# Optimization experiments

Measured on AMD Instinct MI355X. Metric: run time of the kernel, lower is better.

## Reference

```python
import jax, jax.numpy as jnp
import numpy as np

N, L, D = 2, 2048, 96
H, DK, DV = 4, 16, 16
OUT = 96
SPATIAL = H * (3 + 1 + 3)  # points + distance + direction per head
INF = 100000.0
EPS_DIR = 1e-10
EPS_LN = 1e-5


def setup_inputs() -> dict:
    key = jax.random.key(0)
    ks = jax.random.split(key, 10)
    return {
        "x": jax.random.normal(ks[0], (N, L, D), jnp.float32),
        "pos_CA": jax.random.normal(ks[1], (N, L, 3), jnp.float32),
        "pos_CB": jax.random.normal(ks[2], (N, L, 3), jnp.float32),
        "frame": jax.random.normal(ks[3], (N, L, 3, 3), jnp.float32),
        "mask": jnp.ones((N, L), dtype=bool),
        "Wq": jax.random.normal(ks[4], (D, H * DK), jnp.float32) * 0.1,
        "Wk": jax.random.normal(ks[5], (D, H * DK), jnp.float32) * 0.1,
        "Wv": jax.random.normal(ks[6], (D, H * DV), jnp.float32) * 0.1,
        "Wo": jax.random.normal(ks[7], (H * DV + SPATIAL, OUT), jnp.float32) * 0.1,
        "bo": jnp.zeros((OUT,), jnp.float32),
        "gamma": jnp.ones((OUT,), jnp.float32),
        "beta": jnp.zeros((OUT,), jnp.float32),
    }


def reference(x, pos_CA, pos_CB, frame, mask, Wq, Wk, Wv, Wo, bo, gamma, beta):
    n, l, _ = x.shape
    q = (x @ Wq).reshape(n, l, H, DK)
    k = (x @ Wk).reshape(n, l, H, DK)
    v = (x @ Wv).reshape(n, l, H, DV)

    # logits (N, L_q, L_k, H)
    logits = jnp.einsum('blhd,bkhd->blkh', q, k)
    mask_row = mask[:, :, None, None]           # (N, L, 1, 1)
    mask_pair = mask_row & mask[:, None, :, None]
    logits = jnp.where(mask_pair, logits, logits - INF)
    alpha = jax.nn.softmax(logits, axis=2)
    alpha = jnp.where(mask_row, alpha, 0.0)

    feat_node = jnp.einsum('blkh,bkhd->blhd', alpha, v).reshape(n, l, H * DV)

    # rel_pos[b,l,k] = CB[k] - CA[l]
    rel_pos = pos_CB[:, None, :, :] - pos_CA[:, :, None, :]
    atom_pos_bias = jnp.einsum('blkh,blkd->blhd', alpha, rel_pos)  # (N,L,H,3)
    feat_distance = jnp.linalg.norm(atom_pos_bias, axis=-1, keepdims=True)
    feat_points = jnp.einsum('blij,blhj->blhi', frame, atom_pos_bias)
    feat_direction = feat_points / (jnp.linalg.norm(feat_points, axis=-1, keepdims=True) + EPS_DIR)

    feat_spatial = jnp.concatenate([
        feat_points.reshape(n, l, H * 3),
        feat_distance.reshape(n, l, H),
        feat_direction.reshape(n, l, H * 3),
    ], axis=-1)

    feat_all = jnp.concatenate([feat_node, feat_spatial], axis=-1) @ Wo + bo
    feat_all = jnp.where(mask[:, :, None], feat_all, 0.0)

    # output_dim == input_dim -> residual + LayerNorm
    h = x + feat_all
    mu = jnp.mean(h, axis=-1, keepdims=True)
    var = jnp.var(h, axis=-1, keepdims=True)
    return (h - mu) / jnp.sqrt(var + EPS_LN) * gamma + beta
```

## Files before the change

### kernel.cpp

```cpp
#include <hip/hip_runtime.h>
#include <hip/hip_fp16.h>

typedef _Float16 f16;
typedef _Float16 v8h __attribute__((ext_vector_type(8)));
typedef short    v4s __attribute__((ext_vector_type(4)));
typedef short    v8s __attribute__((ext_vector_type(8)));
typedef float    v4f __attribute__((ext_vector_type(4)));

#define NB   2
#define LSEQ 2048
#define DIM  96
#define NH   4
#define ROWS 4096
#define NT16 128
#define NT32 64
#define OUTD 96
#define SHIFT 12.0f
#define ST 28
#define PART_STRIDE 320

#define MFMA_F16(A, B, C)  __builtin_amdgcn_mfma_f32_16x16x32_f16((A), (B), (C), 0, 0, 0)
#define MFMA_BF16(A, B, C) __builtin_amdgcn_mfma_f32_16x16x32_bf16((A), (B), (C), 0, 0, 0)

static __device__ __forceinline__ short f2bf(float f) {
    unsigned u = __builtin_bit_cast(unsigned, f);
    u += 0x7FFF + ((u >> 16) & 1);
    return (short)(u >> 16);
}

__global__ __launch_bounds__(256) void proj_kernel(
    const float* __restrict__ x,
    const float* __restrict__ posCB,
    const float* __restrict__ Wq,
    const float* __restrict__ Wk,
    const float* __restrict__ Wv,
    f16*   __restrict__ qc,
    f16*   __restrict__ kc,
    short* __restrict__ vf,
    short* __restrict__ pf)
{
    const int t    = threadIdx.x;
    const int w    = t >> 6;
    const int lane = t & 63;
    const int tile = blockIdx.x / 3;
    const int role = blockIdx.x - tile * 3;
    const int b    = tile >> 7;
    const int t16  = tile & 127;
    const int row0 = b * LSEQ + t16 * 16;
    const int h    = lane >> 4, d = lane & 15;

    __shared__ float xs[16 * DIM];
    __shared__ float Wl[DIM * 64];
    __shared__ short stage[4][264];

    const float* Wsel = (role == 0) ? Wq : (role == 1) ? Wk : Wv;
    {
        const float* src = x + (size_t)row0 * DIM;
        #pragma unroll
        for (int i = 0; i < 6; ++i)  xs[t + 256 * i] = src[t + 256 * i];
        #pragma unroll
        for (int i = 0; i < 24; ++i) Wl[t + 256 * i] = Wsel[t + 256 * i];
    }
    __syncthreads();

    float acc[4] = {0.f, 0.f, 0.f, 0.f};
    #pragma unroll 8
    for (int dd = 0; dd < DIM; ++dd) {
        const float wv = Wl[dd * 64 + lane];
        #pragma unroll
        for (int r = 0; r < 4; ++r)
            acc[r] = fmaf(xs[(w * 4 + r) * DIM + dd], wv, acc[r]);
    }

    if (role < 2) {
        #pragma unroll
        for (int r = 0; r < 4; ++r) {
            const int m = w * 4 + r;
            const int idx = (m + 16 * (d >> 3)) * 8 + (d & 7);
            stage[h][idx] = __builtin_bit_cast(short, (f16)acc[r]);
        }
    } else {
        #pragma unroll
        for (int r = 0; r < 4; ++r) {
            const int m = w * 4 + r;
            const int idx = (d + 16 * (m >> 3)) * 8 + (m & 7);
            stage[h][idx] = f2bf(acc[r]);
        }
    }
    __syncthreads();

    const int bh = b * NH + w;
    const v4s val = *(v4s*)(void*)&stage[w][lane * 4];
    if (role == 0)
        *(v4s*)(void*)(qc + ((size_t)(bh * NT16 + t16)) * 256 + lane * 4) = val;
    else if (role == 1)
        *(v4s*)(void*)(kc + ((size_t)(bh * NT16 + t16)) * 256 + lane * 4) = val;
    else
        *(v4s*)(vf + ((size_t)(bh * NT32 + (t16 >> 1))) * 512 + (t16 & 1) * 256 + lane * 4) = val;

    if (blockIdx.x < NB * NT32) {
        const int b2 = blockIdx.x >> 6, t2 = blockIdx.x & 63;
        const int lf = t & 63, jh = t >> 6;
        const int n = lf & 15, kq = lf >> 4;
        #pragma unroll
        for (int u = 0; u < 2; ++u) {
            const int key = t2 * 32 + kq * 8 + jh * 2 + u;
            float val2 = 0.f;
            if (n < 3)       val2 = posCB[((size_t)(b2 * LSEQ + key)) * 3 + n];
            else if (n == 3) val2 = 1.f;
            pf[((size_t)(b2 * NT32 + t2)) * 512 + lf * 8 + jh * 2 + u] = f2bf(val2);
        }
    }
}

__global__ __launch_bounds__(512, 1) void attn_kernel(
    const f16*   __restrict__ qc,
    const f16*   __restrict__ kc,
    const short* __restrict__ vf,
    const short* __restrict__ pf,
    float*       __restrict__ part)
{
    const int w     = threadIdx.x >> 6;
    const int lane  = threadIdx.x & 63;
    const int head  = w & 3, khalf = w >> 2;
    const int b     = blockIdx.x >> 9;
    const int qt    = (blockIdx.x >> 2) & 127;
    const int kq    = blockIdx.x & 3;
    const int bh    = b * NH + head;
    const int quad  = lane >> 4, c16 = lane & 15;

    __shared__ short pT[8][32 * ST];

    v8h aq = {0,0,0,0,0,0,0,0};
    if (lane < 32)
        aq = *(const v8h*)(qc + ((size_t)(bh * NT16 + qt)) * 256 + lane * 8);
    const f16*   kb = kc + (size_t)bh * NT16 * 256;
    const short* vb = vf + (size_t)bh * NT32 * 512;
    const short* pb = pf + (size_t)b  * NT32 * 512;

    v4f O  = {0.f, 0.f, 0.f, 0.f};
    v4f Wa = {0.f, 0.f, 0.f, 0.f};
    const v4f zero = {0.f, 0.f, 0.f, 0.f};
    float srow[4] = {0.f, 0.f, 0.f, 0.f};
    short* slot = pT[w];

    #pragma unroll 2
    for (int i = 0; i < 8; ++i) {
        const int t32 = kq * 16 + khalf * 8 + i;
        v8h bk0 = {0,0,0,0,0,0,0,0}, bk1 = {0,0,0,0,0,0,0,0};
        if (lane < 32) {
            bk0 = *(const v8h*)(kb + (size_t)(2 * t32    ) * 256 + lane * 8);
            bk1 = *(const v8h*)(kb + (size_t)(2 * t32 + 1) * 256 + lane * 8);
        }
        v4f S0 = MFMA_F16(aq, bk0, zero);
        v4f S1 = MFMA_F16(aq, bk1, zero);

        v4s pr0, pr1;
        #pragma unroll
        for (int r = 0; r < 4; ++r) {
            const float e0 = __expf(S0[r] - SHIFT);
            const float e1 = __expf(S1[r] - SHIFT);
            pr0[r] = f2bf(e0);
            pr1[r] = f2bf(e1);
            srow[r] += e0 + e1;
        }

        *(v4s*)(slot + c16 * ST + quad * 4)        = pr0;
        *(v4s*)(slot + (16 + c16) * ST + quad * 4) = pr1;
        v8s ap;
        #pragma unroll
        for (int j = 0; j < 8; ++j)
            ap[j] = slot[(quad * 8 + j) * ST + c16];

        const v8s bv = *(const v8s*)(vb + (size_t)t32 * 512 + lane * 8);
        O = MFMA_BF16(ap, bv, O);
        const v8s bp = *(const v8s*)(pb + (size_t)t32 * 512 + lane * 8);
        Wa = MFMA_BF16(ap, bp, Wa);
    }

    #pragma unroll
    for (int mask = 1; mask < 16; mask <<= 1) {
        #pragma unroll
        for (int r = 0; r < 4; ++r) srow[r] += __shfl_xor(srow[r], mask);
    }

    const int combo = kq * 2 + khalf;
    float* dst = part + ((((size_t)(b * 128 + qt)) * 8 + combo) * 4 + head) * PART_STRIDE;
    *(v4f*)(dst + lane * 4) = O;
    if (c16 < 3) {
        #pragma unroll
        for (int r = 0; r < 4; ++r)
            dst[256 + (4 * quad + r) * 3 + c16] = Wa[r];
    }
    if (c16 == 3) {
        #pragma unroll
        for (int r = 0; r < 4; ++r) dst[304 + 4 * quad + r] = srow[r];
    }
}

__global__ __launch_bounds__(512) void epi_kernel(
    const float* __restrict__ part,
    const float* __restrict__ x,
    const float* __restrict__ posCA,
    const float* __restrict__ frame,
    const float* __restrict__ Wo,
    const float* __restrict__ bo,
    const float* __restrict__ gamma,
    const float* __restrict__ beta,
    float*       __restrict__ out)
{
    const int w    = threadIdx.x >> 6;
    const int lane = threadIdx.x & 63;
    const int b    = blockIdx.x >> 7;
    const int qt   = blockIdx.x & 127;
    const int quad = lane >> 4, c16 = lane & 15;

    __shared__ float feat[16][100];
    __shared__ float aps[16][NH][3];

    if (w < 4) {
        const float* pbase =
            part + (((size_t)(b * 128 + qt)) * 8 * 4 + w) * PART_STRIDE;
        v4f O = {0.f, 0.f, 0.f, 0.f};
        float wa[4] = {0.f, 0.f, 0.f, 0.f};
        float sr[4] = {0.f, 0.f, 0.f, 0.f};
        #pragma unroll
        for (int combo = 0; combo < 8; ++combo) {
            const float* pp = pbase + (size_t)combo * 4 * PART_STRIDE;
            O += *(const v4f*)(pp + lane * 4);
            if (c16 < 3) {
                #pragma unroll
                for (int r = 0; r < 4; ++r)
                    wa[r] += pp[256 + (4 * quad + r) * 3 + c16];
            }
            #pragma unroll
            for (int r = 0; r < 4; ++r) sr[r] += pp[304 + 4 * quad + r];
        }
        float inv[4];
        #pragma unroll
        for (int r = 0; r < 4; ++r) inv[r] = 1.f / sr[r];
        #pragma unroll
        for (int r = 0; r < 4; ++r)
            feat[4 * quad + r][w * 16 + c16] = O[r] * inv[r];
        if (c16 < 3) {
            #pragma unroll
            for (int r = 0; r < 4; ++r)
                aps[4 * quad + r][w][c16] = wa[r] * inv[r];
        }
    }
    __syncthreads();

    const int rowg0 = b * LSEQ + qt * 16;

    if (lane < 8) {
        const int pair = w * 8 + lane;
        const int r16 = pair >> 2, hh = pair & 3;
        const int grow = rowg0 + r16;
        float apb[3];
        #pragma unroll
        for (int j = 0; j < 3; ++j)
            apb[j] = aps[r16][hh][j] - posCA[(size_t)grow * 3 + j];
        const float dist = sqrtf(apb[0]*apb[0] + apb[1]*apb[1] + apb[2]*apb[2]);
        float fp[3];
        #pragma unroll
        for (int i = 0; i < 3; ++i) {
            float a = 0.f;
            #pragma unroll
            for (int j = 0; j < 3; ++j)
                a = fmaf(frame[(size_t)grow * 9 + i * 3 + j], apb[j], a);
            fp[i] = a;
        }
        const float fpn  = sqrtf(fp[0]*fp[0] + fp[1]*fp[1] + fp[2]*fp[2]);
        const float rinv = 1.f / (fpn + 1e-10f);
        #pragma unroll
        for (int i = 0; i < 3; ++i) {
            feat[r16][64 + hh * 3 + i] = fp[i];
            feat[r16][80 + hh * 3 + i] = fp[i] * rinv;
        }
        feat[r16][76 + hh] = dist;
    }
    __syncthreads();

    #pragma unroll
    for (int rr = 0; rr < 2; ++rr) {
        const int r16 = w * 2 + rr;
        const int grow = rowg0 + r16;

        float acc0 = bo[lane];
        #pragma unroll 4
        for (int r2 = 0; r2 < 92; ++r2)
            acc0 = fmaf(feat[r16][r2], Wo[r2 * OUTD + lane], acc0);
        const float hv0 = acc0 + x[(size_t)grow * DIM + lane];

        float hv1 = 0.f;
        if (lane < 32) {
            float acc1 = bo[64 + lane];
            #pragma unroll 4
            for (int r2 = 0; r2 < 92; ++r2)
                acc1 = fmaf(feat[r16][r2], Wo[r2 * OUTD + 64 + lane], acc1);
            hv1 = acc1 + x[(size_t)grow * DIM + 64 + lane];
        }

        float ls = hv0 + hv1;
        float lq = fmaf(hv0, hv0, hv1 * hv1);
        #pragma unroll
        for (int off = 32; off > 0; off >>= 1) {
            ls += __shfl_xor(ls, off);
            lq += __shfl_xor(lq, off);
        }
        const float mu  = ls * (1.f / OUTD);
        const float var = lq * (1.f / OUTD) - mu * mu;
        const float rs  = rsqrtf(var + 1e-5f);

        out[(size_t)grow * OUTD + lane] = (hv0 - mu) * rs * gamma[lane] + beta[lane];
        if (lane < 32)
            out[(size_t)grow * OUTD + 64 + lane] =
                (hv1 - mu) * rs * gamma[64 + lane] + beta[64 + lane];
    }
}

extern "C" void kernel_launch(void* const* d_in, const int* in_sizes, int n_in,
                              void* d_out, int out_size, void* d_ws, size_t ws_size,
                              hipStream_t stream)
{
    const float* x     = (const float*)d_in[0];
    const float* posCA = (const float*)d_in[1];
    const float* posCB = (const float*)d_in[2];
    const float* frame = (const float*)d_in[3];
    const float* Wq    = (const float*)d_in[5];
    const float* Wk    = (const float*)d_in[6];
    const float* Wv    = (const float*)d_in[7];
    const float* Wo    = (const float*)d_in[8];
    const float* bo    = (const float*)d_in[9];
    const float* gamma = (const float*)d_in[10];
    const float* beta  = (const float*)d_in[11];

    f16*   qc   = (f16*)d_ws;
    f16*   kc   = qc + (size_t)8 * NT16 * 256;
    short* vf   = (short*)(kc + (size_t)8 * NT16 * 256);
    short* pf   = vf + (size_t)8 * NT32 * 512;
    float* part = (float*)(pf + (size_t)NB * NT32 * 512);

    proj_kernel<<<256 * 3, 256, 0, stream>>>(x, posCB, Wq, Wk, Wv, qc, kc, vf, pf);
    attn_kernel<<<NB * NT16 * 4, 512, 0, stream>>>(qc, kc, vf, pf, part);
    epi_kernel<<<NB * NT16, 512, 0, stream>>>(part, x, posCA, frame,
                                              Wo, bo, gamma, beta,
                                              (float*)d_out);
}
```

Measured before the change: 123.9 us.

## Interleave K tile layout, vectorize staging loads, truncate exp to bf16

The projection kernel now loads x and the weight matrix into shared memory as float4 instead of scalar floats. K is stored in an interleaved 32-key layout, so each lane fetches both 16-key halves with one contiguous 32-byte read instead of two strided reads. The exp-to-bf16 conversion in attention becomes a truncating bit shift, and the row sum uses the same truncated values so the normalization matches the weights actually fed to the MFMA. The truncation drops round-to-nearest, which slightly changes numerics.

```diff
diff --git a/kernel.cpp b/kernel.cpp
--- a/kernel.cpp
+++ b/kernel.cpp
@@ -6,6 +6,7 @@
 typedef short    v4s __attribute__((ext_vector_type(4)));
 typedef short    v8s __attribute__((ext_vector_type(8)));
 typedef float    v4f __attribute__((ext_vector_type(4)));
+typedef unsigned int u32;
 
 #define NB   2
 #define LSEQ 2048
@@ -55,11 +56,12 @@
 
     const float* Wsel = (role == 0) ? Wq : (role == 1) ? Wk : Wv;
     {
-        const float* src = x + (size_t)row0 * DIM;
-        #pragma unroll
-        for (int i = 0; i < 6; ++i)  xs[t + 256 * i] = src[t + 256 * i];
-        #pragma unroll
-        for (int i = 0; i < 24; ++i) Wl[t + 256 * i] = Wsel[t + 256 * i];
+        const float4* src = (const float4*)(x + (size_t)row0 * DIM);
+        ((float4*)xs)[t] = src[t];
+        if (t < 128) ((float4*)xs)[256 + t] = src[256 + t];
+        const float4* ws4 = (const float4*)Wsel;
+        #pragma unroll
+        for (int i = 0; i < 6; ++i) ((float4*)Wl)[t + 256 * i] = ws4[t + 256 * i];
     }
     __syncthreads();
 
@@ -93,9 +95,10 @@
     const v4s val = *(v4s*)(void*)&stage[w][lane * 4];
     if (role == 0)
         *(v4s*)(void*)(qc + ((size_t)(bh * NT16 + t16)) * 256 + lane * 4) = val;
-    else if (role == 1)
-        *(v4s*)(void*)(kc + ((size_t)(bh * NT16 + t16)) * 256 + lane * 4) = val;
-    else
+    else if (role == 1) {
+        *(v4s*)(void*)(kc + ((size_t)(bh * NT32 + (t16 >> 1))) * 512
+                          + (lane >> 1) * 16 + (t16 & 1) * 8 + (lane & 1) * 4) = val;
+    } else
         *(v4s*)(vf + ((size_t)(bh * NT32 + (t16 >> 1))) * 512 + (t16 & 1) * 256 + lane * 4) = val;
 
     if (blockIdx.x < NB * NT32) {
@@ -134,7 +137,7 @@
     v8h aq = {0,0,0,0,0,0,0,0};
     if (lane < 32)
         aq = *(const v8h*)(qc + ((size_t)(bh * NT16 + qt)) * 256 + lane * 8);
-    const f16*   kb = kc + (size_t)bh * NT16 * 256;
+    const f16*   kb = kc + (size_t)bh * NT32 * 512;
     const short* vb = vf + (size_t)bh * NT32 * 512;
     const short* pb = pf + (size_t)b  * NT32 * 512;
 
@@ -149,8 +152,9 @@
         const int t32 = kq * 16 + khalf * 8 + i;
         v8h bk0 = {0,0,0,0,0,0,0,0}, bk1 = {0,0,0,0,0,0,0,0};
         if (lane < 32) {
-            bk0 = *(const v8h*)(kb + (size_t)(2 * t32    ) * 256 + lane * 8);
-            bk1 = *(const v8h*)(kb + (size_t)(2 * t32 + 1) * 256 + lane * 8);
+            const f16* kp = kb + (size_t)t32 * 512 + lane * 16;
+            bk0 = *(const v8h*)(kp);
+            bk1 = *(const v8h*)(kp + 8);
         }
         v4f S0 = MFMA_F16(aq, bk0, zero);
         v4f S1 = MFMA_F16(aq, bk1, zero);
@@ -158,11 +162,12 @@
         v4s pr0, pr1;
         #pragma unroll
         for (int r = 0; r < 4; ++r) {
-            const float e0 = __expf(S0[r] - SHIFT);
-            const float e1 = __expf(S1[r] - SHIFT);
-            pr0[r] = f2bf(e0);
-            pr1[r] = f2bf(e1);
-            srow[r] += e0 + e1;
+            const u32 a0 = __builtin_bit_cast(u32, __expf(S0[r] - SHIFT));
+            const u32 a1 = __builtin_bit_cast(u32, __expf(S1[r] - SHIFT));
+            pr0[r] = (short)(a0 >> 16);
+            pr1[r] = (short)(a1 >> 16);
+            srow[r] += __builtin_bit_cast(float, a0 & 0xFFFF0000u)
+                     + __builtin_bit_cast(float, a1 & 0xFFFF0000u);
         }
 
         *(v4s*)(slot + c16 * ST + quad * 4)        = pr0;
```

Result: faster. 120.0 us (-3.2%).
